# Performance work log

Measured on AMD Instinct MI355X. Metric: run time of the kernel, lower is better.

The kernel has to match this reference:

```python
import jax, jax.numpy as jnp
import numpy as np

N_NODES, N_EDGES, N_GRAPHS, N_FEATS = 100000, 1600000, 256, 128
BN_EPS = 1e-5


def setup_inputs() -> dict:
    key = jax.random.key(0)
    ks = jax.random.split(key, 12)
    x = jax.random.normal(ks[0], (N_NODES, N_FEATS), jnp.float32)
    edge_index = jax.random.randint(ks[1], (2, N_EDGES), 0, N_NODES, dtype=jnp.int64)
    batch = jnp.sort(jax.random.randint(ks[2], (N_NODES,), 0, N_GRAPHS, dtype=jnp.int64))
    s = 0.05
    return {
        "x": x,
        "edge_index": edge_index,
        "batch": batch,
        "W1": jax.random.normal(ks[3], (N_FEATS, 32), jnp.float32) * s,
        "b1": jnp.zeros((32,), jnp.float32),
        "W2": jax.random.normal(ks[4], (32, 64), jnp.float32) * s,
        "b2": jnp.zeros((64,), jnp.float32),
        "fcW1": jax.random.normal(ks[5], (64, 32), jnp.float32) * s,
        "fcb1": jnp.zeros((32,), jnp.float32),
        "gamma": jnp.ones((32,), jnp.float32),
        "beta": jnp.zeros((32,), jnp.float32),
        "fcW2": jax.random.normal(ks[6], (32, 1), jnp.float32) * s,
        "fcb2": jnp.zeros((1,), jnp.float32),
    }


def _gcn_conv(x, src, dst, deg_inv, W, b):
    # PyG GCNConv: h = x @ W; out[d] = sum_e norm_e * h[src_e] + self-loop + b
    h = x @ W  # [N, out]
    norm = deg_inv[src] * deg_inv[dst]  # [E]
    msg = h[src] * norm[:, None]
    out = jax.ops.segment_sum(msg, dst, num_segments=x.shape[0])
    out = out + (deg_inv * deg_inv)[:, None] * h  # self-loop contribution
    return out + b


def reference(x, edge_index, batch, W1, b1, W2, b2, fcW1, fcb1, gamma, beta, fcW2, fcb2):
    src, dst = edge_index[0], edge_index[1]
    n = x.shape[0]
    # degree with self loops, computed on target nodes (PyG default)
    deg = 1.0 + jax.ops.segment_sum(jnp.ones_like(src, dtype=x.dtype), dst, num_segments=n)
    deg_inv = jax.lax.rsqrt(deg)
    h = _gcn_conv(x, src, dst, deg_inv, W1, b1)   # [N, 32]
    h = _gcn_conv(h, src, dst, deg_inv, W2, b2)   # [N, 64]
    # scatter_mean over graph batch
    sums = jax.ops.segment_sum(h, batch, num_segments=N_GRAPHS)  # [G, 64]
    cnt = jax.ops.segment_sum(jnp.ones((n,), h.dtype), batch, num_segments=N_GRAPHS)
    pooled = sums / jnp.maximum(cnt, 1.0)[:, None]
    # head: Linear -> ReLU -> BatchNorm1d (batch stats) -> Dropout(eval=id) -> Linear -> Softplus
    z = jax.nn.relu(pooled @ fcW1 + fcb1)  # [G, 32]
    mu = jnp.mean(z, axis=0)
    var = jnp.var(z, axis=0)
    z = (z - mu) * jax.lax.rsqrt(var + BN_EPS) * gamma + beta
    out = jax.nn.softplus(z @ fcW2 + fcb2)  # [G, 1]
    return out
```

## Files before the change

kernel.cpp:

```cpp
#include <hip/hip_runtime.h>

#define NN 100000
#define NE 1600000
#define NG 256

#define BSH 8
#define NPB 256
#define NBKT ((NN + NPB - 1) / NPB)
#define TILE 8192
#define NB_P1 ((NE + TILE - 1) / TILE)

__device__ __forceinline__ unsigned short f2bf(float x) {
    unsigned int u = __float_as_uint(x);
    u += 0x7FFFu + ((u >> 16) & 1u);
    return (unsigned short)(u >> 16);
}
__device__ __forceinline__ float2 bf2x2(unsigned int v) {
    float2 r;
    r.x = __uint_as_float(v << 16);
    r.y = __uint_as_float(v & 0xFFFF0000u);
    return r;
}
__device__ __forceinline__ unsigned int bfpack(float x, float y) {
    return (unsigned int)f2bf(x) | ((unsigned int)f2bf(y) << 16);
}

__global__ __launch_bounds__(1024) void count_kernel(const int* __restrict__ dst,
                                                     int* __restrict__ bkt_cnt) {
    __shared__ int hist[NBKT];
    int tid = threadIdx.x;
    int e0 = blockIdx.x * TILE;
    int e1 = min(e0 + TILE, NE);
    for (int i = tid; i < NBKT; i += 1024) hist[i] = 0;
    __syncthreads();
    for (int e = e0 + tid; e < e1; e += 1024)
        atomicAdd(&hist[dst[e] >> BSH], 1);
    __syncthreads();
    for (int i = tid; i < NBKT; i += 1024) {
        int h = hist[i];
        if (h) atomicAdd(&bkt_cnt[i], h);
    }
}

__global__ __launch_bounds__(1024) void scan_bkt_kernel(const int* __restrict__ bkt_cnt,
                                                        int* __restrict__ bkt_ptr,
                                                        int* __restrict__ bkt_cur) {
    __shared__ int ts[1024];
    int tid = threadIdx.x;
    int v = (tid < NBKT) ? bkt_cnt[tid] : 0;
    ts[tid] = v;
    __syncthreads();
    for (int off = 1; off < 1024; off <<= 1) {
        int t = (tid >= off) ? ts[tid - off] : 0;
        __syncthreads();
        ts[tid] += t;
        __syncthreads();
    }
    if (tid < NBKT) {
        int base = ts[tid] - v;
        bkt_ptr[tid] = base;
        bkt_cur[tid] = base;
    }
    if (tid == 0) bkt_ptr[NBKT] = NE;
}

__global__ __launch_bounds__(1024) void part_kernel(const int* __restrict__ src,
                                                    const int* __restrict__ dst,
                                                    int* __restrict__ bkt_cur,
                                                    int* __restrict__ epack) {
    __shared__ int hist[NBKT];
    __shared__ int cur[NBKT];
    int tid = threadIdx.x;
    int e0 = blockIdx.x * TILE;
    int e1 = min(e0 + TILE, NE);
    for (int i = tid; i < NBKT; i += 1024) hist[i] = 0;
    __syncthreads();
    for (int e = e0 + tid; e < e1; e += 1024)
        atomicAdd(&hist[dst[e] >> BSH], 1);
    __syncthreads();
    for (int i = tid; i < NBKT; i += 1024) {
        int h = hist[i];
        cur[i] = h ? atomicAdd(&bkt_cur[i], h) : 0;
    }
    __syncthreads();
    for (int e = e0 + tid; e < e1; e += 1024) {
        int d = dst[e];
        int pos = atomicAdd(&cur[d >> BSH], 1);
        epack[pos] = src[e] | ((d & (NPB - 1)) << 17);
    }
}

__global__ __launch_bounds__(256) void build_kernel(const int* __restrict__ epack,
                                                    const int* __restrict__ bkt_ptr,
                                                    int* __restrict__ row_ptr,
                                                    int* __restrict__ col,
                                                    float* __restrict__ deg_inv) {
    __shared__ int cnt[NPB];
    __shared__ int ts[NPB];
    int b = blockIdx.x;
    int tid = threadIdx.x;
    int ebase = bkt_ptr[b], eend = bkt_ptr[b + 1];
    int nbase = b << BSH;
    cnt[tid] = 0;
    __syncthreads();
    for (int e = ebase + tid; e < eend; e += 256)
        atomicAdd(&cnt[epack[e] >> 17], 1);
    __syncthreads();
    int v = cnt[tid];
    ts[tid] = v;
    __syncthreads();
    for (int off = 1; off < NPB; off <<= 1) {
        int t = (tid >= off) ? ts[tid - off] : 0;
        __syncthreads();
        ts[tid] += t;
        __syncthreads();
    }
    {
        int loff = ts[tid] - v;
        int node = nbase + tid;
        if (node < NN) {
            row_ptr[node] = ebase + loff;
            deg_inv[node] = rsqrtf(1.0f + (float)v);
        }
        cnt[tid] = loff;
    }
    if (b == 0 && tid == 0) row_ptr[NN] = NE;
    __syncthreads();
    for (int e = ebase + tid; e < eend; e += 256) {
        int rec = epack[e];
        int r = atomicAdd(&cnt[rec >> 17], 1);
        col[ebase + r] = rec & 0x1FFFF;
    }
}

__global__ __launch_bounds__(256) void gemm_x_w1(const float* __restrict__ x,
                                                 const float* __restrict__ W,
                                                 const float* __restrict__ deg_inv,
                                                 unsigned short* __restrict__ h, int N) {
    __shared__ float wsh[128 * 32];
    __shared__ float xs[32][132];
    int tid = threadIdx.x;
    int row0 = blockIdx.x * 32;
    for (int i = tid; i < 1024; i += 256)
        ((float4*)wsh)[i] = ((const float4*)W)[i];
    for (int i = tid; i < 1024; i += 256) {
        int r = i >> 5, c4 = i & 31;
        *(float4*)&xs[r][c4 * 4] = ((const float4*)(x + (size_t)(row0 + r) * 128))[c4];
    }
    __syncthreads();
    int r = tid >> 3;
    int c8 = (tid & 7) * 4;
    float acc0 = 0.f, acc1 = 0.f, acc2 = 0.f, acc3 = 0.f;
#pragma unroll
    for (int k0 = 0; k0 < 128; k0 += 4) {
        float4 xv = *(const float4*)&xs[r][k0];
#pragma unroll
        for (int j = 0; j < 4; ++j) {
            float xk = (&xv.x)[j];
            float4 wv = *(const float4*)&wsh[(k0 + j) * 32 + c8];
            acc0 += xk * wv.x;
            acc1 += xk * wv.y;
            acc2 += xk * wv.z;
            acc3 += xk * wv.w;
        }
    }
    float di = deg_inv[row0 + r];
    ushort4 o;
    o.x = f2bf(acc0 * di);
    o.y = f2bf(acc1 * di);
    o.z = f2bf(acc2 * di);
    o.w = f2bf(acc3 * di);
    *(ushort4*)&h[(size_t)(row0 + r) * 32 + c8] = o;
}

template <int MODE>
__global__ __launch_bounds__(256) void conv_bf_kernel(const int* __restrict__ row_ptr,
                                                      const int* __restrict__ col,
                                                      const uint2* __restrict__ h2,
                                                      const float* __restrict__ deg_inv,
                                                      const float* __restrict__ b,
                                                      uint2* __restrict__ out_bf,
                                                      float4* __restrict__ out_f32) {
    int gid = blockIdx.x * blockDim.x + threadIdx.x;
    int node = gid >> 3;
    int L = gid & 7;
    if (node >= NN) return;
    int beg = row_ptr[node], end = row_ptr[node + 1];
    uint2 sv = h2[node * 8 + L];
    float2 s0 = bf2x2(sv.x), s1 = bf2x2(sv.y);
    float a00 = s0.x, a01 = s0.y, a02 = s1.x, a03 = s1.y;
    float a10 = 0.f, a11 = 0.f, a12 = 0.f, a13 = 0.f;
    float a20 = 0.f, a21 = 0.f, a22 = 0.f, a23 = 0.f;
    float a30 = 0.f, a31 = 0.f, a32 = 0.f, a33 = 0.f;
    for (int j0 = beg; j0 < end; j0 += 8) {
        int idx = j0 + L;
        int myc = (idx < end) ? col[idx] : 0;
        int m = end - j0;
        if (m > 8) m = 8;
        int t = 0;
        for (; t + 4 <= m; t += 4) {
            int c0 = __shfl(myc, t, 8);
            int c1 = __shfl(myc, t + 1, 8);
            int c2 = __shfl(myc, t + 2, 8);
            int c3 = __shfl(myc, t + 3, 8);
            uint2 v0 = h2[c0 * 8 + L];
            uint2 v1 = h2[c1 * 8 + L];
            uint2 v2 = h2[c2 * 8 + L];
            uint2 v3 = h2[c3 * 8 + L];
            float2 p0 = bf2x2(v0.x), q0 = bf2x2(v0.y);
            float2 p1 = bf2x2(v1.x), q1 = bf2x2(v1.y);
            float2 p2 = bf2x2(v2.x), q2 = bf2x2(v2.y);
            float2 p3 = bf2x2(v3.x), q3 = bf2x2(v3.y);
            a00 += p0.x; a01 += p0.y; a02 += q0.x; a03 += q0.y;
            a10 += p1.x; a11 += p1.y; a12 += q1.x; a13 += q1.y;
            a20 += p2.x; a21 += p2.y; a22 += q2.x; a23 += q2.y;
            a30 += p3.x; a31 += p3.y; a32 += q3.x; a33 += q3.y;
        }
        for (; t < m; ++t) {
            int c = __shfl(myc, t, 8);
            uint2 v = h2[c * 8 + L];
            float2 p = bf2x2(v.x), q = bf2x2(v.y);
            a00 += p.x; a01 += p.y; a02 += q.x; a03 += q.y;
        }
    }
    float c0 = (a00 + a10) + (a20 + a30);
    float c1 = (a01 + a11) + (a21 + a31);
    float c2 = (a02 + a12) + (a22 + a32);
    float c3 = (a03 + a13) + (a23 + a33);
    float di = deg_inv[node];
    if (MODE == 0) {
        float o0 = di * di * c0 + di * b[4 * L];
        float o1 = di * di * c1 + di * b[4 * L + 1];
        float o2 = di * di * c2 + di * b[4 * L + 2];
        float o3 = di * di * c3 + di * b[4 * L + 3];
        out_bf[node * 8 + L] = make_uint2(bfpack(o0, o1), bfpack(o2, o3));
    } else {
        out_f32[node * 8 + L] = make_float4(di * c0, di * c1, di * c2, di * c3);
    }
}

__global__ void pool_kernel(const float* __restrict__ h, const int* __restrict__ batch,
                            float* __restrict__ gsum, float* __restrict__ gcnt, int N) {
    int t = blockIdx.x * blockDim.x + threadIdx.x;
    int chunk = t / 32;
    int f = t % 32;
    int n0 = chunk * 16;
    if (n0 >= N) return;
    int n1 = min(n0 + 16, N);
    int cur = batch[n0];
    float acc = 0.f, ccnt = 0.f;
    for (int n = n0; n < n1; ++n) {
        int b = batch[n];
        if (b != cur) {
            unsafeAtomicAdd(&gsum[cur * 32 + f], acc);
            if (f == 0) unsafeAtomicAdd(&gcnt[cur], ccnt);
            acc = 0.f; ccnt = 0.f; cur = b;
        }
        acc += h[(size_t)n * 32 + f];
        ccnt += 1.f;
    }
    unsafeAtomicAdd(&gsum[cur * 32 + f], acc);
    if (f == 0) unsafeAtomicAdd(&gcnt[cur], ccnt);
}

__global__ __launch_bounds__(256) void head_kernel(const float* __restrict__ gsum,
                                                   const float* __restrict__ gcnt,
                                                   const float* __restrict__ W2,
                                                   const float* __restrict__ b2,
                                                   const float* __restrict__ fcW1,
                                                   const float* __restrict__ fcb1,
                                                   const float* __restrict__ gamma,
                                                   const float* __restrict__ beta,
                                                   const float* __restrict__ fcW2,
                                                   const float* __restrict__ fcb2,
                                                   float* __restrict__ out) {
    __shared__ float zs[NG][33];
    __shared__ float wcs[32 * 32];
    __shared__ float bcs[32];
    __shared__ float part1[8][32];
    __shared__ float part2[8][32];
    __shared__ float mu[32], rstd[32];
    int g = threadIdx.x;

    for (int idx = g; idx < 32 * 32; idx += 256) {
        int k = idx / 32, ch = idx % 32;
        float a = 0.f;
#pragma unroll
        for (int j = 0; j < 64; ++j) a += W2[k * 64 + j] * fcW1[j * 32 + ch];
        wcs[idx] = a;
    }
    if (g < 32) {
        float a = fcb1[g];
#pragma unroll
        for (int j = 0; j < 64; ++j) a += b2[j] * fcW1[j * 32 + g];
        bcs[g] = a;
    }
    __syncthreads();

    float p32[32];
    float inv = 1.0f / fmaxf(gcnt[g], 1.0f);
    {
        const float4* gs4 = (const float4*)(gsum + g * 32);
#pragma unroll
        for (int q = 0; q < 8; ++q) {
            float4 v = gs4[q];
            p32[q * 4 + 0] = v.x * inv;
            p32[q * 4 + 1] = v.y * inv;
            p32[q * 4 + 2] = v.z * inv;
            p32[q * 4 + 3] = v.w * inv;
        }
    }
#pragma unroll 4
    for (int ch = 0; ch < 32; ++ch) {
        float acc = bcs[ch];
#pragma unroll
        for (int k = 0; k < 32; ++k) acc += p32[k] * wcs[k * 32 + ch];
        zs[g][ch] = fmaxf(acc, 0.f);
    }
    __syncthreads();

    {
        int ch = g & 31, seg = g >> 5;
        float s = 0.f, sq = 0.f;
#pragma unroll
        for (int i = 0; i < 32; ++i) {
            float v = zs[seg * 32 + i][ch];
            s += v;
            sq += v * v;
        }
        part1[seg][ch] = s;
        part2[seg][ch] = sq;
    }
    __syncthreads();
    if (g < 32) {
        float s = 0.f, sq = 0.f;
#pragma unroll
        for (int i = 0; i < 8; ++i) { s += part1[i][g]; sq += part2[i][g]; }
        float m = s / NG;
        float v = sq / NG - m * m;
        mu[g] = m;
        rstd[g] = rsqrtf(fmaxf(v, 0.f) + 1e-5f);
    }
    __syncthreads();

    float acc = fcb2[0];
#pragma unroll 4
    for (int ch = 0; ch < 32; ++ch) {
        float zn = (zs[g][ch] - mu[ch]) * rstd[ch] * gamma[ch] + beta[ch];
        acc += zn * fcW2[ch];
    }
    out[g] = fmaxf(acc, 0.f) + log1pf(expf(-fabsf(acc)));
}

extern "C" void kernel_launch(void* const* d_in, const int* in_sizes, int n_in,
                              void* d_out, int out_size, void* d_ws, size_t ws_size,
                              hipStream_t stream) {
    const float* x     = (const float*)d_in[0];
    const int*   ei    = (const int*)d_in[1];
    const int*   batch = (const int*)d_in[2];
    const float* W1    = (const float*)d_in[3];
    const float* b1    = (const float*)d_in[4];
    const float* W2    = (const float*)d_in[5];
    const float* b2    = (const float*)d_in[6];
    const float* fcW1  = (const float*)d_in[7];
    const float* fcb1  = (const float*)d_in[8];
    const float* gamma = (const float*)d_in[9];
    const float* beta  = (const float*)d_in[10];
    const float* fcW2  = (const float*)d_in[11];
    const float* fcb2  = (const float*)d_in[12];
    float* out = (float*)d_out;

    char* p = (char*)d_ws;
    int*   bkt_cnt = (int*)p;        p += 400 * 4;
    int*   bkt_ptr = (int*)p;        p += 400 * 4;
    int*   bkt_cur = (int*)p;        p += 400 * 4;
    float* deg_inv = (float*)p;      p += (size_t)NN * 4;
    int*   row_ptr = (int*)p;        p += (size_t)(NN + 8) * 4;
    int*   epack   = (int*)p;        p += (size_t)NE * 4;
    int*   col     = (int*)p;        p += (size_t)NE * 4;
    unsigned short* h1s = (unsigned short*)p;  p += (size_t)NN * 32 * 2;
    uint2*          t1  = (uint2*)p;           p += (size_t)NN * 8 * 8;
    float* agg2    = (float*)p;      p += (size_t)NN * 32 * 4;
    float* gsum    = (float*)p;      p += (size_t)NG * 32 * 4;
    float* gcnt    = (float*)p;      p += (size_t)NG * 4;

    const int* srcv = ei;
    const int* dstv = ei + NE;

    hipMemsetAsync(bkt_cnt, 0, NBKT * sizeof(int), stream);
    hipMemsetAsync(gsum, 0, (NG * 32 + NG) * sizeof(float), stream);

    count_kernel<<<NB_P1, 1024, 0, stream>>>(dstv, bkt_cnt);
    scan_bkt_kernel<<<1, 1024, 0, stream>>>(bkt_cnt, bkt_ptr, bkt_cur);
    part_kernel<<<NB_P1, 1024, 0, stream>>>(srcv, dstv, bkt_cur, epack);
    build_kernel<<<NBKT, 256, 0, stream>>>(epack, bkt_ptr, row_ptr, col, deg_inv);

    gemm_x_w1<<<NN / 32, 256, 0, stream>>>(x, W1, deg_inv, h1s, NN);
    conv_bf_kernel<0><<<((size_t)NN * 8 + 255) / 256, 256, 0, stream>>>(
        row_ptr, col, (const uint2*)h1s, deg_inv, b1, t1, nullptr);

    conv_bf_kernel<1><<<((size_t)NN * 8 + 255) / 256, 256, 0, stream>>>(
        row_ptr, col, (const uint2*)t1, deg_inv, b1, nullptr, (float4*)agg2);

    pool_kernel<<<(((NN + 15) / 16) * 32 + 255) / 256, 256, 0, stream>>>(agg2, batch, gsum, gcnt, NN);
    head_kernel<<<1, 256, 0, stream>>>(gsum, gcnt, W2, b2, fcW1, fcb1, gamma, beta, fcW2, fcb2, out);
}
```

Baseline: 259.4 us.

## Bin nodes by degree and process conv kernels in degree-sorted order

```diff
diff --git a/kernel.cpp b/kernel.cpp
--- a/kernel.cpp
+++ b/kernel.cpp
@@ -9,6 +9,7 @@
 #define NBKT ((NN + NPB - 1) / NPB)
 #define TILE 8192
 #define NB_P1 ((NE + TILE - 1) / TILE)
+#define NBIN 16
 
 __device__ __forceinline__ unsigned short f2bf(float x) {
     unsigned int u = __float_as_uint(x);
@@ -94,14 +95,17 @@
                                                     const int* __restrict__ bkt_ptr,
                                                     int* __restrict__ row_ptr,
                                                     int* __restrict__ col,
-                                                    float* __restrict__ deg_inv) {
+                                                    float* __restrict__ deg_inv,
+                                                    int* __restrict__ bin_cnt) {
     __shared__ int cnt[NPB];
     __shared__ int ts[NPB];
+    __shared__ int bhist[NBIN];
     int b = blockIdx.x;
     int tid = threadIdx.x;
     int ebase = bkt_ptr[b], eend = bkt_ptr[b + 1];
     int nbase = b << BSH;
     cnt[tid] = 0;
+    if (tid < NBIN) bhist[tid] = 0;
     __syncthreads();
     for (int e = ebase + tid; e < eend; e += 256)
         atomicAdd(&cnt[epack[e] >> 17], 1);
@@ -121,16 +125,47 @@
         if (node < NN) {
             row_ptr[node] = ebase + loff;
             deg_inv[node] = rsqrtf(1.0f + (float)v);
+            atomicAdd(&bhist[min(v >> 3, NBIN - 1)], 1);
         }
         cnt[tid] = loff;
     }
     if (b == 0 && tid == 0) row_ptr[NN] = NE;
     __syncthreads();
+    if (tid < NBIN && bhist[tid]) atomicAdd(&bin_cnt[tid], bhist[tid]);
     for (int e = ebase + tid; e < eend; e += 256) {
         int rec = epack[e];
         int r = atomicAdd(&cnt[rec >> 17], 1);
         col[ebase + r] = rec & 0x1FFFF;
     }
+}
+
+__global__ void scan16_kernel(const int* __restrict__ bin_cnt, int* __restrict__ bin_cur) {
+    if (threadIdx.x == 0) {
+        int s = 0;
+        for (int i = 0; i < NBIN; ++i) { bin_cur[i] = s; s += bin_cnt[i]; }
+    }
+}
+
+__global__ __launch_bounds__(256) void place_kernel(const int* __restrict__ row_ptr,
+                                                    int* __restrict__ bin_cur,
+                                                    int* __restrict__ perm) {
+    __shared__ int bhist[NBIN];
+    __shared__ int bbase[NBIN];
+    int b = blockIdx.x, tid = threadIdx.x;
+    int node = (b << BSH) + tid;
+    bool valid = node < NN;
+    int bin = 0, rank = 0;
+    if (tid < NBIN) bhist[tid] = 0;
+    __syncthreads();
+    if (valid) {
+        int deg = row_ptr[node + 1] - row_ptr[node];
+        bin = min(deg >> 3, NBIN - 1);
+        rank = atomicAdd(&bhist[bin], 1);
+    }
+    __syncthreads();
+    if (tid < NBIN) bbase[tid] = bhist[tid] ? atomicAdd(&bin_cur[tid], bhist[tid]) : 0;
+    __syncthreads();
+    if (valid) perm[bbase[bin] + rank] = node;
 }
 
 __global__ __launch_bounds__(256) void gemm_x_w1(const float* __restrict__ x,
@@ -174,7 +209,8 @@
 }
 
 template <int MODE>
-__global__ __launch_bounds__(256) void conv_bf_kernel(const int* __restrict__ row_ptr,
+__global__ __launch_bounds__(256) void conv_bf_kernel(const int* __restrict__ perm,
+                                                      const int* __restrict__ row_ptr,
                                                       const int* __restrict__ col,
                                                       const uint2* __restrict__ h2,
                                                       const float* __restrict__ deg_inv,
@@ -182,9 +218,10 @@
                                                       uint2* __restrict__ out_bf,
                                                       float4* __restrict__ out_f32) {
     int gid = blockIdx.x * blockDim.x + threadIdx.x;
-    int node = gid >> 3;
+    int g8 = gid >> 3;
     int L = gid & 7;
-    if (node >= NN) return;
+    if (g8 >= NN) return;
+    int node = perm[g8];
     int beg = row_ptr[node], end = row_ptr[node + 1];
     uint2 sv = h2[node * 8 + L];
     float2 s0 = bf2x2(sv.x), s1 = bf2x2(sv.y);
@@ -372,10 +409,13 @@
 
     char* p = (char*)d_ws;
     int*   bkt_cnt = (int*)p;        p += 400 * 4;
+    int*   bin_cnt = (int*)p;        p += 16 * 4;
+    int*   bin_cur = (int*)p;        p += 16 * 4;
     int*   bkt_ptr = (int*)p;        p += 400 * 4;
     int*   bkt_cur = (int*)p;        p += 400 * 4;
     float* deg_inv = (float*)p;      p += (size_t)NN * 4;
     int*   row_ptr = (int*)p;        p += (size_t)(NN + 8) * 4;
+    int*   perm    = (int*)p;        p += (size_t)NN * 4;
     int*   epack   = (int*)p;        p += (size_t)NE * 4;
     int*   col     = (int*)p;        p += (size_t)NE * 4;
     unsigned short* h1s = (unsigned short*)p;  p += (size_t)NN * 32 * 2;
@@ -387,20 +427,23 @@
     const int* srcv = ei;
     const int* dstv = ei + NE;
 
-    hipMemsetAsync(bkt_cnt, 0, NBKT * sizeof(int), stream);
+    hipMemsetAsync(bkt_cnt, 0, (400 + 16) * sizeof(int), stream);
     hipMemsetAsync(gsum, 0, (NG * 32 + NG) * sizeof(float), stream);
 
     count_kernel<<<NB_P1, 1024, 0, stream>>>(dstv, bkt_cnt);
     scan_bkt_kernel<<<1, 1024, 0, stream>>>(bkt_cnt, bkt_ptr, bkt_cur);
     part_kernel<<<NB_P1, 1024, 0, stream>>>(srcv, dstv, bkt_cur, epack);
-    build_kernel<<<NBKT, 256, 0, stream>>>(epack, bkt_ptr, row_ptr, col, deg_inv);
+    build_kernel<<<NBKT, 256, 0, stream>>>(epack, bkt_ptr, row_ptr, col, deg_inv, bin_cnt);
+
+    scan16_kernel<<<1, 64, 0, stream>>>(bin_cnt, bin_cur);
+    place_kernel<<<NBKT, 256, 0, stream>>>(row_ptr, bin_cur, perm);
 
     gemm_x_w1<<<NN / 32, 256, 0, stream>>>(x, W1, deg_inv, h1s, NN);
     conv_bf_kernel<0><<<((size_t)NN * 8 + 255) / 256, 256, 0, stream>>>(
-        row_ptr, col, (const uint2*)h1s, deg_inv, b1, t1, nullptr);
+        perm, row_ptr, col, (const uint2*)h1s, deg_inv, b1, t1, nullptr);
 
     conv_bf_kernel<1><<<((size_t)NN * 8 + 255) / 256, 256, 0, stream>>>(
-        row_ptr, col, (const uint2*)t1, deg_inv, b1, nullptr, (float4*)agg2);
+        perm, row_ptr, col, (const uint2*)t1, deg_inv, b1, nullptr, (float4*)agg2);
 
     pool_kernel<<<(((NN + 15) / 16) * 32 + 255) / 256, 256, 0, stream>>>(agg2, batch, gsum, gcnt, NN);
     head_kernel<<<1, 256, 0, stream>>>(gsum, gcnt, W2, b2, fcW1, fcb1, gamma, beta, fcW2, fcb2, out);
```

Result: slower. 270.4 us (+4.3%).
